# Performance work log

Hardware: AMD Instinct MI355X
Metric: run time of the kernel (lower is better)

The kernel has to match this reference:

```python
import jax, jax.numpy as jnp
import numpy as np

N_DATA = 128      # number of datasets (process conditions)
SEG_LEN = 131072  # thickness points per dataset
N_MAT = 8         # number of distinct materials
N_MATP = 8        # material params: Sigma0, BetaD, Ea, Mfda, Di, A0, B0, l0
N_PROCP = 5       # process params: SigmaC, K0, alpha1, L0, GrainSize_200
RGAS = 8.314      # gas constant, J/(mol K)


def setup_inputs() -> dict:
    key = jax.random.key(0)
    k1, k2, k3, k4 = jax.random.split(key, 4)
    # thickness points: sorted within each dataset segment, scaled to [0, 1]
    x = jax.random.uniform(k1, (N_DATA, SEG_LEN), dtype=jnp.float32)
    x_scaled = jnp.sort(x, axis=1).reshape(-1)
    # process conditions [R, T, P, Melting_T]
    pc = jax.random.uniform(k2, (N_DATA, 4), dtype=jnp.float32)
    R = 0.05 + pc[:, 0]            # deposition rate
    T = 300.0 + 300.0 * pc[:, 1]   # temperature (K)
    P = 0.1 + pc[:, 2]             # pressure
    material_index = jnp.sort(jax.random.randint(k3, (N_DATA,), 0, N_MAT, dtype=jnp.int32))
    melting_T = 1000.0 + 100.0 * material_index.astype(jnp.float32)
    process_c = jnp.stack([R, T, P, melting_T], axis=1)
    # learned raw parameters (pre-sigmoid) and bounds
    n_params = N_MAT * N_MATP + N_DATA * N_PROCP  # 704
    raw_params = 0.5 * jax.random.normal(k4, (n_params,), dtype=jnp.float32)
    para_lb = jnp.full((n_params,), 0.1, dtype=jnp.float32)
    para_ub = jnp.full((n_params,), 2.0, dtype=jnp.float32)
    # MinMaxScaler surrogates: [x_data_min, x_data_max, y_data_min, y_data_max], feature_range=(0,1)
    scaler_params = jnp.array([0.5, 500.0, -50.0, 50.0], dtype=jnp.float32)
    fit_index = jnp.repeat(jnp.arange(1, N_DATA + 1, dtype=jnp.int32), SEG_LEN)
    return {
        'x_scaled': x_scaled, 'process_c': process_c, 'raw_params': raw_params,
        'para_lb': para_lb, 'para_ub': para_ub, 'scaler_params': scaler_params,
        'fit_index': fit_index, 'material_index': material_index,
    }


def _stress(tp, R, T, P, SigmaC, alpha1, L0, G200, Sigma0, BetaD, Ea, Mfda, Di, A0, B0, l0):
    """Kinetic stress equation (Chason-type). tp: [N, L-1]; params broadcast [N, 1]."""
    Lg = G200 * (tp / 200.0 + 1e-3) ** alpha1 + L0      # grain size evolution
    D = Di * jnp.exp(-Ea / (RGAS * T))                   # thermally activated diffusivity
    beta = BetaD * D / (R * Lg + 1e-9)                   # kinetic competition factor
    sigma_ss = (SigmaC - Mfda * P + (Sigma0 / Lg) * beta) / (1.0 + beta)
    return sigma_ss + A0 * jnp.exp(-tp / (B0 * l0 + 1e-9))  # steady-state + transient


def reference(x_scaled, process_c, raw_params, para_lb, para_ub, scaler_params,
              fit_index, material_index):
    n_data = process_c.shape[0]
    seg = x_scaled.shape[0] // n_data
    # unscale parameters: sigmoid -> [lb, ub]
    xv = jax.nn.sigmoid(raw_params) * (para_ub - para_lb) + para_lb
    materials = xv[:N_MAT * N_MATP].reshape(N_MAT, N_MATP)
    process = xv[N_MAT * N_MATP:].reshape(n_data, N_PROCP)
    x_min, x_max, y_min, y_max = scaler_params[0], scaler_params[1], scaler_params[2], scaler_params[3]
    # inverse MinMax transform of thickness (feature_range = (0, 1))
    t = (x_scaled * (x_max - x_min) + x_min).reshape(n_data, seg)  # [N, L]
    SigmaC, K0, alpha1, L0, G200 = (process[:, i:i + 1] for i in range(5))
    mat = materials[material_index]  # [N, 8] gather per-dataset material params
    Sigma0, BetaD, Ea, Mfda, Di, A0, B0, l0 = (mat[:, i:i + 1] for i in range(8))
    R, T, P = process_c[:, 0:1], process_c[:, 1:2], process_c[:, 2:3]
    # Euler integration: Fit[j+1] = Fit[j] + stress(t[j]) * dT  ==  K0 + cumsum
    s = _stress(t[:, :-1], R, T, P, SigmaC, alpha1, L0, G200,
                Sigma0, BetaD, Ea, Mfda, Di, A0, B0, l0)   # [N, L-1]
    dT = jnp.diff(t, axis=1)                                # [N, L-1]
    fit = jnp.concatenate([K0, K0 + jnp.cumsum(s * dT, axis=1)], axis=1).reshape(-1)
    # forward MinMax transform of stress-thickness (feature_range = (0, 1))
    return (fit - y_min) / (y_max - y_min)
```

## Files before the change

kernel.cpp:

```cpp
#include <hip/hip_runtime.h>

#define N_DATA   128
#define SEG_LEN  131072
#define NPROD    (SEG_LEN - 1)
#define N_MAT    8
#define N_MATP   8
#define N_PROCP  5
#define RGAS     8.314f

#define NCH      64
#define CHUNK    2048
#define TPB      256
#define EPT      8

typedef float nt4 __attribute__((ext_vector_type(4)));

__device__ __forceinline__ float stress_s(float t,
    float alpha1, float L0, float G200, float Sigma0, float A0,
    float inv_tau, float cbd, float base_num, float R) {
  float Lg  = G200 * __expf(alpha1 * __logf(t * (1.0f / 200.0f) + 0.001f)) + L0;
  float u   = R * Lg + 1e-9f;
  float num = base_num * u * Lg + Sigma0 * cbd;
  float den = Lg * (u + cbd);
  float sigma_ss = num * __builtin_amdgcn_rcpf(den);
  return sigma_ss + A0 * __expf(-t * inv_tau);
}

__global__ __launch_bounds__(TPB) void k1_sums(
    const float* __restrict__ x,
    const float* __restrict__ pc, const float* __restrict__ raw,
    const float* __restrict__ lb, const float* __restrict__ ub,
    const float* __restrict__ sc, const int* __restrict__ mat_idx,
    float* __restrict__ chunksum) {
  __shared__ float pv[13];
  __shared__ float ws4[4];

  int b   = blockIdx.x;
  int row = b >> 6;
  int ch  = b & (NCH - 1);
  int tid = threadIdx.x;
  int lane = tid & 63, wv = tid >> 6;

  long rowbase = (long)row * SEG_LEN;
  int  gb = ch * CHUNK + tid * EPT;
  const float* xp = x + rowbase + gb;
  float4 a  = *(const float4*)xp;
  float4 bq = *(const float4*)(xp + 4);
  float  xn = (gb + EPT < SEG_LEN) ? xp[EPT] : 0.0f;

  if (tid < 13) {
    int idx = (tid < 5) ? (N_MAT * N_MATP + row * N_PROCP + tid)
                        : (mat_idx[row] * N_MATP + (tid - 5));
    float s = 1.0f / (1.0f + __expf(-raw[idx]));
    pv[tid] = s * (ub[idx] - lb[idx]) + lb[idx];
  }
  __syncthreads();

  float SigmaC = pv[0], alpha1 = pv[2], L0 = pv[3], G200 = pv[4];
  float Sigma0 = pv[5], BetaD = pv[6], Ea = pv[7], Mfda = pv[8], Di = pv[9];
  float A0 = pv[10], B0 = pv[11], l0 = pv[12];
  float R = pc[row * 4 + 0], T = pc[row * 4 + 1], P = pc[row * 4 + 2];
  float cbd      = BetaD * Di * __expf(-Ea / (RGAS * T));
  float base_num = SigmaC - Mfda * P;
  float inv_tau  = 1.0f / (B0 * l0 + 1e-9f);
  float x_min = sc[0], x_sc = sc[1] - sc[0];

  float tv[9];
  tv[0] = a.x  * x_sc + x_min; tv[1] = a.y  * x_sc + x_min;
  tv[2] = a.z  * x_sc + x_min; tv[3] = a.w  * x_sc + x_min;
  tv[4] = bq.x * x_sc + x_min; tv[5] = bq.y * x_sc + x_min;
  tv[6] = bq.z * x_sc + x_min; tv[7] = bq.w * x_sc + x_min;
  tv[8] = xn   * x_sc + x_min;

  float sum = 0.0f;
#pragma unroll
  for (int k = 0; k < EPT; k++) {
    if (gb + k < NPROD) {
      float s = stress_s(tv[k], alpha1, L0, G200, Sigma0, A0, inv_tau, cbd, base_num, R);
      sum += s * (tv[k + 1] - tv[k]);
    }
  }

#pragma unroll
  for (int d = 32; d > 0; d >>= 1) sum += __shfl_down(sum, d);
  if (lane == 0) ws4[wv] = sum;
  __syncthreads();
  if (tid == 0) chunksum[b] = ws4[0] + ws4[1] + ws4[2] + ws4[3];
}

__global__ __launch_bounds__(TPB) void k2_write(
    const float* __restrict__ x,
    const float* __restrict__ pc, const float* __restrict__ raw,
    const float* __restrict__ lb, const float* __restrict__ ub,
    const float* __restrict__ sc, const int* __restrict__ mat_idx,
    const float* __restrict__ chunksum,
    float* __restrict__ out) {
  __shared__ float pv[13];
  __shared__ float wtot[4];

  int b   = blockIdx.x;
  int row = b >> 6;
  int ch  = b & (NCH - 1);
  int tid = threadIdx.x;
  int lane = tid & 63, wv = tid >> 6;

  long rowbase = (long)row * SEG_LEN;
  int  gb = ch * CHUNK + tid * EPT;
  const float* xp = x + rowbase + gb;
  float4 a  = *(const float4*)xp;
  float4 bq = *(const float4*)(xp + 4);
  float  xn = (gb + EPT < SEG_LEN) ? xp[EPT] : 0.0f;
  float csv = chunksum[(row << 6) | lane];

  if (tid < 13) {
    int idx = (tid < 5) ? (N_MAT * N_MATP + row * N_PROCP + tid)
                        : (mat_idx[row] * N_MATP + (tid - 5));
    float s = 1.0f / (1.0f + __expf(-raw[idx]));
    pv[tid] = s * (ub[idx] - lb[idx]) + lb[idx];
  }

  float cincl = csv;
#pragma unroll
  for (int d = 1; d < 64; d <<= 1) {
    float n = __shfl_up(cincl, d);
    if (lane >= d) cincl += n;
  }
  float choff = __shfl(cincl - csv, ch);

  __syncthreads();
  float SigmaC = pv[0], K0 = pv[1], alpha1 = pv[2], L0 = pv[3], G200 = pv[4];
  float Sigma0 = pv[5], BetaD = pv[6], Ea = pv[7], Mfda = pv[8], Di = pv[9];
  float A0 = pv[10], B0 = pv[11], l0 = pv[12];
  float R = pc[row * 4 + 0], T = pc[row * 4 + 1], P = pc[row * 4 + 2];
  float cbd      = BetaD * Di * __expf(-Ea / (RGAS * T));
  float base_num = SigmaC - Mfda * P;
  float inv_tau  = 1.0f / (B0 * l0 + 1e-9f);
  float x_min = sc[0], x_sc = sc[1] - sc[0];
  float y_min = sc[2], inv_yr = 1.0f / (sc[3] - sc[2]);

  float tv[9];
  tv[0] = a.x  * x_sc + x_min; tv[1] = a.y  * x_sc + x_min;
  tv[2] = a.z  * x_sc + x_min; tv[3] = a.w  * x_sc + x_min;
  tv[4] = bq.x * x_sc + x_min; tv[5] = bq.y * x_sc + x_min;
  tv[6] = bq.z * x_sc + x_min; tv[7] = bq.w * x_sc + x_min;
  tv[8] = xn   * x_sc + x_min;

  float pref[EPT];
  float run = 0.0f;
#pragma unroll
  for (int k = 0; k < EPT; k++) {
    float p = 0.0f;
    if (gb + k < NPROD) {
      float s = stress_s(tv[k], alpha1, L0, G200, Sigma0, A0, inv_tau, cbd, base_num, R);
      p = s * (tv[k + 1] - tv[k]);
    }
    run += p;
    pref[k] = run;
  }

  float incl = run;
#pragma unroll
  for (int d = 1; d < 64; d <<= 1) {
    float n = __shfl_up(incl, d);
    if (lane >= d) incl += n;
  }
  if (lane == 63) wtot[wv] = incl;
  __syncthreads();
  float low = 0.0f;
#pragma unroll
  for (int w = 0; w < 4; w++) low += (w < wv) ? wtot[w] : 0.0f;

  float base = K0 + choff + (incl - run) + low;
  nt4 o0, o1;
  o0.x = (base           - y_min) * inv_yr;
  o0.y = (base + pref[0] - y_min) * inv_yr;
  o0.z = (base + pref[1] - y_min) * inv_yr;
  o0.w = (base + pref[2] - y_min) * inv_yr;
  o1.x = (base + pref[3] - y_min) * inv_yr;
  o1.y = (base + pref[4] - y_min) * inv_yr;
  o1.z = (base + pref[5] - y_min) * inv_yr;
  o1.w = (base + pref[6] - y_min) * inv_yr;
  nt4* op = (nt4*)(out + rowbase + gb);
  __builtin_nontemporal_store(o0, op);
  __builtin_nontemporal_store(o1, op + 1);
}

extern "C" void kernel_launch(void* const* d_in, const int* in_sizes, int n_in,
                              void* d_out, int out_size, void* d_ws, size_t ws_size,
                              hipStream_t stream) {
  const float* x_scaled  = (const float*)d_in[0];
  const float* process_c = (const float*)d_in[1];
  const float* raw       = (const float*)d_in[2];
  const float* lb        = (const float*)d_in[3];
  const float* ub        = (const float*)d_in[4];
  const float* sc        = (const float*)d_in[5];
  const int*   mat_idx   = (const int*)d_in[7];
  float* out = (float*)d_out;
  float* chunksum = (float*)d_ws;

  k1_sums<<<N_DATA * NCH, TPB, 0, stream>>>(
      x_scaled, process_c, raw, lb, ub, sc, mat_idx, chunksum);
  k2_write<<<N_DATA * NCH, TPB, 0, stream>>>(
      x_scaled, process_c, raw, lb, ub, sc, mat_idx, chunksum, out);
}
```

Measured before the change: 180.2 us.

## Fold scaling constants into per-row coefficients, use exp2/log2, and double elements per thread

Folds the input min-max rescale and output scaling into precomputed per-row coefficients so the per-element math runs on raw x values and writes scaled outputs directly. It switches to hardware exp2/log2 intrinsics to avoid base conversions. It also doubles the work per thread (16 elements, 32 chunks per row), which halves the block count and shrinks the chunk-offset scan to 32 lanes. The folding changes the floating-point rounding order slightly, and the larger register arrays may lower occupancy.

```diff
diff --git a/kernel.cpp b/kernel.cpp
--- a/kernel.cpp
+++ b/kernel.cpp
@@ -7,23 +7,56 @@
 #define N_MATP   8
 #define N_PROCP  5
 #define RGAS     8.314f
-
-#define NCH      64
-#define CHUNK    2048
+#define LOG2E    1.44269504f
+
+#define NCH      32
+#define CHUNK    4096
 #define TPB      256
-#define EPT      8
+#define EPT      16
 
 typedef float nt4 __attribute__((ext_vector_type(4)));
 
-__device__ __forceinline__ float stress_s(float t,
-    float alpha1, float L0, float G200, float Sigma0, float A0,
-    float inv_tau, float cbd, float base_num, float R) {
-  float Lg  = G200 * __expf(alpha1 * __logf(t * (1.0f / 200.0f) + 0.001f)) + L0;
-  float u   = R * Lg + 1e-9f;
-  float num = base_num * u * Lg + Sigma0 * cbd;
-  float den = Lg * (u + cbd);
-  float sigma_ss = num * __builtin_amdgcn_rcpf(den);
-  return sigma_ss + A0 * __expf(-t * inv_tau);
+#define amd_exp2(x) __builtin_amdgcn_exp2f(x)
+#define amd_log2(x) __builtin_amdgcn_logf(x)
+
+struct RowK {
+  float c_la, c_lb, alpha1, L0, G200, R, cbd, bn_s, s0cbd_s, A0_s, c_ea, c_eb, K0_s;
+};
+
+__device__ __forceinline__ RowK derive(const float pv[13],
+    const float* __restrict__ pc, const float* __restrict__ sc, int row) {
+  RowK k;
+  float SigmaC = pv[0], K0 = pv[1];
+  k.alpha1 = pv[2]; k.L0 = pv[3]; k.G200 = pv[4];
+  float Sigma0 = pv[5], BetaD = pv[6], Ea = pv[7], Mfda = pv[8], Di = pv[9];
+  float A0 = pv[10], B0 = pv[11], l0 = pv[12];
+  k.R = pc[row * 4 + 0];
+  float T = pc[row * 4 + 1], P = pc[row * 4 + 2];
+  float x_min = sc[0], x_sc = sc[1] - sc[0];
+  float y_min = sc[2], inv_yr = 1.0f / (sc[3] - sc[2]);
+  float S = x_sc * inv_yr;
+  k.cbd     = BetaD * Di * __expf(-Ea / (RGAS * T));
+  k.bn_s    = (SigmaC - Mfda * P) * S;
+  k.s0cbd_s = Sigma0 * k.cbd * S;
+  float inv_tau = 1.0f / (B0 * l0 + 1e-9f);
+  k.A0_s    = A0 * S;
+  k.c_la    = x_sc * (1.0f / 200.0f);
+  k.c_lb    = x_min * (1.0f / 200.0f) + 0.001f;
+  k.c_ea    = -x_sc * inv_tau * LOG2E;
+  k.c_eb    = -x_min * inv_tau * LOG2E;
+  k.K0_s    = (K0 - y_min) * inv_yr;
+  return k;
+}
+
+__device__ __forceinline__ float sprod(float xk, float xk1, const RowK& c) {
+  float zl  = xk * c.c_la + c.c_lb;
+  float Lg  = c.G200 * amd_exp2(c.alpha1 * amd_log2(zl)) + c.L0;
+  float u   = c.R * Lg + 1e-9f;
+  float num = c.bn_s * (u * Lg) + c.s0cbd_s;
+  float den = Lg * (u + c.cbd);
+  float e   = amd_exp2(xk * c.c_ea + c.c_eb);
+  float s   = num * __builtin_amdgcn_rcpf(den) + c.A0_s * e;
+  return s * (xk1 - xk);
 }
 
 __global__ __launch_bounds__(TPB) void k1_sums(
@@ -36,7 +69,7 @@
   __shared__ float ws4[4];
 
   int b   = blockIdx.x;
-  int row = b >> 6;
+  int row = b >> 5;
   int ch  = b & (NCH - 1);
   int tid = threadIdx.x;
   int lane = tid & 63, wv = tid >> 6;
@@ -44,9 +77,12 @@
   long rowbase = (long)row * SEG_LEN;
   int  gb = ch * CHUNK + tid * EPT;
   const float* xp = x + rowbase + gb;
-  float4 a  = *(const float4*)xp;
-  float4 bq = *(const float4*)(xp + 4);
-  float  xn = (gb + EPT < SEG_LEN) ? xp[EPT] : 0.0f;
+  float xv[EPT + 1];
+  { float4 q0 = *(const float4*)xp;       xv[0]=q0.x; xv[1]=q0.y; xv[2]=q0.z; xv[3]=q0.w;
+    float4 q1 = *(const float4*)(xp + 4); xv[4]=q1.x; xv[5]=q1.y; xv[6]=q1.z; xv[7]=q1.w;
+    float4 q2 = *(const float4*)(xp + 8); xv[8]=q2.x; xv[9]=q2.y; xv[10]=q2.z; xv[11]=q2.w;
+    float4 q3 = *(const float4*)(xp +12); xv[12]=q3.x; xv[13]=q3.y; xv[14]=q3.z; xv[15]=q3.w;
+    xv[16] = (gb + EPT < SEG_LEN) ? xp[EPT] : 0.0f; }
 
   if (tid < 13) {
     int idx = (tid < 5) ? (N_MAT * N_MATP + row * N_PROCP + tid)
@@ -55,31 +91,12 @@
     pv[tid] = s * (ub[idx] - lb[idx]) + lb[idx];
   }
   __syncthreads();
-
-  float SigmaC = pv[0], alpha1 = pv[2], L0 = pv[3], G200 = pv[4];
-  float Sigma0 = pv[5], BetaD = pv[6], Ea = pv[7], Mfda = pv[8], Di = pv[9];
-  float A0 = pv[10], B0 = pv[11], l0 = pv[12];
-  float R = pc[row * 4 + 0], T = pc[row * 4 + 1], P = pc[row * 4 + 2];
-  float cbd      = BetaD * Di * __expf(-Ea / (RGAS * T));
-  float base_num = SigmaC - Mfda * P;
-  float inv_tau  = 1.0f / (B0 * l0 + 1e-9f);
-  float x_min = sc[0], x_sc = sc[1] - sc[0];
-
-  float tv[9];
-  tv[0] = a.x  * x_sc + x_min; tv[1] = a.y  * x_sc + x_min;
-  tv[2] = a.z  * x_sc + x_min; tv[3] = a.w  * x_sc + x_min;
-  tv[4] = bq.x * x_sc + x_min; tv[5] = bq.y * x_sc + x_min;
-  tv[6] = bq.z * x_sc + x_min; tv[7] = bq.w * x_sc + x_min;
-  tv[8] = xn   * x_sc + x_min;
+  RowK c = derive(pv, pc, sc, row);
 
   float sum = 0.0f;
 #pragma unroll
-  for (int k = 0; k < EPT; k++) {
-    if (gb + k < NPROD) {
-      float s = stress_s(tv[k], alpha1, L0, G200, Sigma0, A0, inv_tau, cbd, base_num, R);
-      sum += s * (tv[k + 1] - tv[k]);
-    }
-  }
+  for (int k = 0; k < EPT; k++)
+    if (gb + k < NPROD) sum += sprod(xv[k], xv[k + 1], c);
 
 #pragma unroll
   for (int d = 32; d > 0; d >>= 1) sum += __shfl_down(sum, d);
@@ -99,7 +116,7 @@
   __shared__ float wtot[4];
 
   int b   = blockIdx.x;
-  int row = b >> 6;
+  int row = b >> 5;
   int ch  = b & (NCH - 1);
   int tid = threadIdx.x;
   int lane = tid & 63, wv = tid >> 6;
@@ -107,10 +124,13 @@
   long rowbase = (long)row * SEG_LEN;
   int  gb = ch * CHUNK + tid * EPT;
   const float* xp = x + rowbase + gb;
-  float4 a  = *(const float4*)xp;
-  float4 bq = *(const float4*)(xp + 4);
-  float  xn = (gb + EPT < SEG_LEN) ? xp[EPT] : 0.0f;
-  float csv = chunksum[(row << 6) | lane];
+  float xv[EPT + 1];
+  { float4 q0 = *(const float4*)xp;       xv[0]=q0.x; xv[1]=q0.y; xv[2]=q0.z; xv[3]=q0.w;
+    float4 q1 = *(const float4*)(xp + 4); xv[4]=q1.x; xv[5]=q1.y; xv[6]=q1.z; xv[7]=q1.w;
+    float4 q2 = *(const float4*)(xp + 8); xv[8]=q2.x; xv[9]=q2.y; xv[10]=q2.z; xv[11]=q2.w;
+    float4 q3 = *(const float4*)(xp +12); xv[12]=q3.x; xv[13]=q3.y; xv[14]=q3.z; xv[15]=q3.w;
+    xv[16] = (gb + EPT < SEG_LEN) ? xp[EPT] : 0.0f; }
+  float csv = chunksum[(row << 5) | (lane & 31)];
 
   if (tid < 13) {
     int idx = (tid < 5) ? (N_MAT * N_MATP + row * N_PROCP + tid)
@@ -121,39 +141,20 @@
 
   float cincl = csv;
 #pragma unroll
-  for (int d = 1; d < 64; d <<= 1) {
+  for (int d = 1; d < 32; d <<= 1) {
     float n = __shfl_up(cincl, d);
-    if (lane >= d) cincl += n;
+    if ((lane & 31) >= d) cincl += n;
   }
   float choff = __shfl(cincl - csv, ch);
 
   __syncthreads();
-  float SigmaC = pv[0], K0 = pv[1], alpha1 = pv[2], L0 = pv[3], G200 = pv[4];
-  float Sigma0 = pv[5], BetaD = pv[6], Ea = pv[7], Mfda = pv[8], Di = pv[9];
-  float A0 = pv[10], B0 = pv[11], l0 = pv[12];
-  float R = pc[row * 4 + 0], T = pc[row * 4 + 1], P = pc[row * 4 + 2];
-  float cbd      = BetaD * Di * __expf(-Ea / (RGAS * T));
-  float base_num = SigmaC - Mfda * P;
-  float inv_tau  = 1.0f / (B0 * l0 + 1e-9f);
-  float x_min = sc[0], x_sc = sc[1] - sc[0];
-  float y_min = sc[2], inv_yr = 1.0f / (sc[3] - sc[2]);
-
-  float tv[9];
-  tv[0] = a.x  * x_sc + x_min; tv[1] = a.y  * x_sc + x_min;
-  tv[2] = a.z  * x_sc + x_min; tv[3] = a.w  * x_sc + x_min;
-  tv[4] = bq.x * x_sc + x_min; tv[5] = bq.y * x_sc + x_min;
-  tv[6] = bq.z * x_sc + x_min; tv[7] = bq.w * x_sc + x_min;
-  tv[8] = xn   * x_sc + x_min;
+  RowK c = derive(pv, pc, sc, row);
 
   float pref[EPT];
   float run = 0.0f;
 #pragma unroll
   for (int k = 0; k < EPT; k++) {
-    float p = 0.0f;
-    if (gb + k < NPROD) {
-      float s = stress_s(tv[k], alpha1, L0, G200, Sigma0, A0, inv_tau, cbd, base_num, R);
-      p = s * (tv[k + 1] - tv[k]);
-    }
+    float p = (gb + k < NPROD) ? sprod(xv[k], xv[k + 1], c) : 0.0f;
     run += p;
     pref[k] = run;
   }
@@ -170,19 +171,18 @@
 #pragma unroll
   for (int w = 0; w < 4; w++) low += (w < wv) ? wtot[w] : 0.0f;
 
-  float base = K0 + choff + (incl - run) + low;
-  nt4 o0, o1;
-  o0.x = (base           - y_min) * inv_yr;
-  o0.y = (base + pref[0] - y_min) * inv_yr;
-  o0.z = (base + pref[1] - y_min) * inv_yr;
-  o0.w = (base + pref[2] - y_min) * inv_yr;
-  o1.x = (base + pref[3] - y_min) * inv_yr;
-  o1.y = (base + pref[4] - y_min) * inv_yr;
-  o1.z = (base + pref[5] - y_min) * inv_yr;
-  o1.w = (base + pref[6] - y_min) * inv_yr;
+  float base = c.K0_s + choff + (incl - run) + low;
   nt4* op = (nt4*)(out + rowbase + gb);
-  __builtin_nontemporal_store(o0, op);
-  __builtin_nontemporal_store(o1, op + 1);
+#pragma unroll
+  for (int j = 0; j < EPT / 4; j++) {
+    int m = j * 4;
+    nt4 o;
+    o.x = (m == 0) ? base : base + pref[m - 1];
+    o.y = base + pref[m + 0];
+    o.z = base + pref[m + 1];
+    o.w = base + pref[m + 2];
+    __builtin_nontemporal_store(o, op + j);
+  }
 }
 
 extern "C" void kernel_launch(void* const* d_in, const int* in_sizes, int n_in,
```

New measurement: 205.3 us. 14.0% more time.
